# Kernel optimization log

Hardware: AMD Instinct MI355X
Metric: run time of the kernel (lower is better)

Reference implementation:

```python
import jax, jax.numpy as jnp
import numpy as np

EPS = 1e-12
SIMILARITY = 'dot'  # non-tensor forward arg, closed over


def setup_inputs() -> dict:
    key = jax.random.key(0)
    k1, k2, k3, k4 = jax.random.split(key, 4)
    N, M, D = 4096, 8192, 512
    x = jax.random.normal(k1, (N, D), dtype=jnp.float32)
    x_n = jax.random.normal(k2, (M, D), dtype=jnp.float32)
    # Linear(D, 3) params
    W = jax.random.normal(k3, (3, D), dtype=jnp.float32) * (1.0 / np.sqrt(D))
    bias = jax.random.normal(k4, (3,), dtype=jnp.float32) * 0.01
    return {"x": x, "x_n": x_n, "W": W, "bias": bias}


def _sim_matrix(x, x_n, similarity):
    if similarity == 'l2':
        d2 = (jnp.sum(x * x, 1)[:, None] - 2.0 * (x @ x_n.T)
              + jnp.sum(x_n * x_n, 1)[None, :])
        return -jnp.sqrt(jnp.maximum(d2, 0.0))
    elif similarity == 'l1':
        return -jnp.sum(jnp.abs(x[:, None, :] - x_n[None, :, :]), axis=-1)
    elif similarity == 'dot':
        return (x @ x_n.T) / x.shape[1]
    elif similarity == 'cos':
        xn = x / jnp.linalg.norm(x, axis=1, keepdims=True)
        yn = x_n / jnp.linalg.norm(x_n, axis=1, keepdims=True)
        return xn @ yn.T


def reference(x, x_n, W, bias):
    # pointwise params from a Linear(D,3)+Sigmoid head, clamped to (eps, 1-eps)
    p = jnp.clip(jax.nn.sigmoid(x @ W.T + bias), EPS, 1.0 - EPS)  # [N,3]
    a = p[:, 0:1]
    b = p[:, 1:2]
    s = p[:, 2:3]
    b = a + b * (1.0 - a)

    sim = _sim_matrix(x, x_n, SIMILARITY)                # [N,M]
    smin = jnp.min(sim, axis=1, keepdims=True)
    smax = jnp.max(sim, axis=1, keepdims=True)
    sim_norm = (sim - smin) / (smax - smin)

    # x != x_n -> plain row max (torch.equal branch is False)
    top_sims = jnp.max(sim_norm, axis=1, keepdims=True)  # [N,1]
    a = jnp.minimum(a, top_sims) - EPS

    num = jnp.maximum(jnp.abs(sim_norm - a) ** (1.0 / s), EPS)
    denom = num + jnp.maximum(jnp.abs(b - sim_norm) ** (1.0 / s), EPS)
    soft_mask = num / denom

    lo = sim_norm < a
    hi = sim_norm > b
    soft_mask = jnp.where(lo, 0.0, jnp.where(hi, 1.0, soft_mask))
    # safe log: masked-to-0 entries give -inf forward, zero grad (matches torch)
    safe = jnp.where(lo, 1.0, soft_mask)
    log_mask = jnp.where(lo, -jnp.inf, jnp.log(safe))
    return sim + log_mask
```

## Files before the change

### kernel.cpp

```cpp
#include <hip/hip_runtime.h>
#include <hip/hip_fp16.h>
#include <math.h>

#define EPSF 1e-12f
#define NEG_HUGE (-1e30f)

typedef _Float16 half8_t __attribute__((ext_vector_type(8)));
typedef _Float16 half4_t __attribute__((ext_vector_type(4)));
typedef float floatx4 __attribute__((ext_vector_type(4)));

__device__ __forceinline__ float sigmoid_stable(float v) {
    if (v >= 0.0f) {
        return 1.0f / (1.0f + expf(-v));
    } else {
        float e = expf(v);
        return e / (1.0f + e);
    }
}

__global__ __launch_bounds__(64) void row_params_kernel(
    const float* __restrict__ x, const float* __restrict__ W,
    const float* __restrict__ bias,
    float* __restrict__ aeff, float* __restrict__ bnew, float* __restrict__ tinv)
{
    const int r = blockIdx.x;
    const int l = threadIdx.x;
    const float* xr = x + (size_t)r * 512;
    float s0 = 0.0f, s1 = 0.0f, s2 = 0.0f;
#pragma unroll
    for (int i = 0; i < 8; ++i) {
        int e = l * 8 + i;
        float xv = xr[e];
        s0 = fmaf(xv, W[e], s0);
        s1 = fmaf(xv, W[512 + e], s1);
        s2 = fmaf(xv, W[1024 + e], s2);
    }
#pragma unroll
    for (int off = 32; off > 0; off >>= 1) {
        s0 += __shfl_xor(s0, off);
        s1 += __shfl_xor(s1, off);
        s2 += __shfl_xor(s2, off);
    }
    if (l == 0) {
        float p0 = fminf(fmaxf(sigmoid_stable(s0 + bias[0]), EPSF), 1.0f);
        float p1 = fminf(fmaxf(sigmoid_stable(s1 + bias[1]), EPSF), 1.0f);
        float p2 = fminf(fmaxf(sigmoid_stable(s2 + bias[2]), EPSF), 1.0f);
        float b = p0 + p1 * (1.0f - p0);
        float ae = fminf(p0, 1.0f) - EPSF;
        aeff[r] = ae;
        bnew[r] = b;
        tinv[r] = 1.0f / p2;
    }
}

__global__ __launch_bounds__(256) void split_gates_kernel(
    const float* __restrict__ x, const float* __restrict__ xn,
    const float* __restrict__ W, const float* __restrict__ bias,
    _Float16* __restrict__ A2, _Float16* __restrict__ B2,
    float* __restrict__ aeff, float* __restrict__ bnew, float* __restrict__ tinv)
{
    __shared__ float sred[3][4];
    int idx = blockIdx.x * 256 + threadIdx.x;
    int row = idx >> 7;
    int c = (idx & 127) << 2;
    const float* src;
    _Float16* dst;
    bool isB;
    if (row < 4096) {
        src = x + (size_t)row * 512 + c;
        dst = A2 + (size_t)row * 1536 + c;
        isB = false;
    } else {
        int r = row - 4096;
        src = xn + (size_t)r * 512 + c;
        dst = B2 + (size_t)r * 1536 + c;
        isB = true;
    }
    float4 v = *(const float4*)src;
    _Float16 h0 = (_Float16)v.x, h1 = (_Float16)v.y,
             h2 = (_Float16)v.z, h3 = (_Float16)v.w;
    half4_t hv = {h0, h1, h2, h3};
    half4_t lv = {(_Float16)(v.x - (float)h0), (_Float16)(v.y - (float)h1),
                  (_Float16)(v.z - (float)h2), (_Float16)(v.w - (float)h3)};
    *(half4_t*)(dst) = hv;
    *(half4_t*)(dst + 512)  = isB ? lv : hv;
    *(half4_t*)(dst + 1024) = isB ? hv : lv;

    if (!isB) {
        float s0 = v.x * W[c] + v.y * W[c + 1] + v.z * W[c + 2] + v.w * W[c + 3];
        float s1 = v.x * W[512 + c] + v.y * W[513 + c]
                 + v.z * W[514 + c] + v.w * W[515 + c];
        float s2 = v.x * W[1024 + c] + v.y * W[1025 + c]
                 + v.z * W[1026 + c] + v.w * W[1027 + c];
#pragma unroll
        for (int off = 32; off > 0; off >>= 1) {
            s0 += __shfl_xor(s0, off);
            s1 += __shfl_xor(s1, off);
            s2 += __shfl_xor(s2, off);
        }
        const int w = threadIdx.x >> 6;
        if ((threadIdx.x & 63) == 0) {
            sred[0][w] = s0; sred[1][w] = s1; sred[2][w] = s2;
        }
        __syncthreads();
        if ((threadIdx.x & 127) == 0) {
            const int w0 = threadIdx.x >> 6;
            float t0 = sred[0][w0] + sred[0][w0 + 1];
            float t1 = sred[1][w0] + sred[1][w0 + 1];
            float t2 = sred[2][w0] + sred[2][w0 + 1];
            float p0 = fminf(fmaxf(sigmoid_stable(t0 + bias[0]), EPSF), 1.0f);
            float p1 = fminf(fmaxf(sigmoid_stable(t1 + bias[1]), EPSF), 1.0f);
            float p2 = fminf(fmaxf(sigmoid_stable(t2 + bias[2]), EPSF), 1.0f);
            float b = p0 + p1 * (1.0f - p0);
            aeff[row] = fminf(p0, 1.0f) - EPSF;
            bnew[row] = b;
            tinv[row] = 1.0f / p2;
        }
    }
}

#define VMW_(N) asm volatile("s_waitcnt vmcnt(" #N ")" ::: "memory")
#define VMW(N) VMW_(N)
#define BARR() __builtin_amdgcn_s_barrier()

__device__ __forceinline__ void gload16(const _Float16* g, _Float16* l) {
    __builtin_amdgcn_global_load_lds(
        (const __attribute__((address_space(1))) unsigned int*)g,
        (__attribute__((address_space(3))) unsigned int*)l, 16, 0, 0);
}

#define RD_A4(dst, QQ, qd)                                                      \
    dst[0] = *(const half8_t*)(lds + (QQ)*16384 + ArdW + (2*(qd))*1024 + g0);   \
    dst[1] = *(const half8_t*)(lds + (QQ)*16384 + ArdW + (2*(qd))*1024 + g1);   \
    dst[2] = *(const half8_t*)(lds + (QQ)*16384 + ArdW + (2*(qd)+1)*1024 + g0); \
    dst[3] = *(const half8_t*)(lds + (QQ)*16384 + ArdW + (2*(qd)+1)*1024 + g1);

#define RD_B8(dst, QQ)                                                          \
    _Pragma("unroll")                                                           \
    for (int fn = 0; fn < 4; ++fn) {                                            \
        dst[2*fn]   = *(const half8_t*)(lds + (QQ)*16384 + BrdW + fn*1024 + g0);\
        dst[2*fn+1] = *(const half8_t*)(lds + (QQ)*16384 + BrdW + fn*1024 + g1);\
    }

#define MFMA_Q(qd, af, bf)                                                      \
    __builtin_amdgcn_s_setprio(1);                                              \
    _Pragma("unroll")                                                           \
    for (int fn = 0; fn < 4; ++fn) {                                            \
        acc[2*(qd)][fn] = __builtin_amdgcn_mfma_f32_16x16x32_f16(               \
            af[0], bf[2*fn], acc[2*(qd)][fn], 0, 0, 0);                         \
        acc[2*(qd)+1][fn] = __builtin_amdgcn_mfma_f32_16x16x32_f16(             \
            af[2], bf[2*fn], acc[2*(qd)+1][fn], 0, 0, 0);                       \
    }                                                                           \
    _Pragma("unroll")                                                           \
    for (int fn = 0; fn < 4; ++fn) {                                            \
        acc[2*(qd)][fn] = __builtin_amdgcn_mfma_f32_16x16x32_f16(               \
            af[1], bf[2*fn+1], acc[2*(qd)][fn], 0, 0, 0);                       \
        acc[2*(qd)+1][fn] = __builtin_amdgcn_mfma_f32_16x16x32_f16(             \
            af[3], bf[2*fn+1], acc[2*(qd)+1][fn], 0, 0, 0);                     \
    }                                                                           \
    __builtin_amdgcn_s_setprio(0);

__global__ __launch_bounds__(512, 2) void mfma_gemm256_kernel(
    const _Float16* __restrict__ A, const _Float16* __restrict__ B,
    float* __restrict__ C,
    float* __restrict__ pmin, float* __restrict__ pmax)
{
    constexpr int KP = 1536;
    constexpr int NN = 8192;
    __shared__ __align__(16) _Float16 lds[65536];

    const int tid = threadIdx.x;
    const int wave = tid >> 6, lane = tid & 63;
    const int bx = blockIdx.x;
    const int by = blockIdx.y;
    const int wm = (wave >> 2) * 128;
    const int wn = (wave & 3) * 64;

    const int rl = lane & 15, lq = lane >> 4;
    const int rx7 = lane & 7;
    const int lrow = lane >> 3, gph = lane & 7;
    const int glog = gph ^ lrow;

    const _Float16* Bg = B + (size_t)(bx * 256 + wave * 8 + lrow) * KP + glog * 8;
    const _Float16* Ag = A + (size_t)(by * 256 + ((wave & 4) ? 128 : 0)
                                      + (wave & 3) * 8 + lrow) * KP + glog * 8;
    const int BdstW = 32768 + (wave * 8) * 64;
    const int AdstW = (((wave & 4) ? 128 : 0) + (wave & 3) * 8) * 64;
    const int ArdW = (wm + rl) * 64;
    const int BrdW = 32768 + (wn + rl) * 64;
    const int g0 = (lq ^ rx7) * 8;
    const int g1 = ((4 + lq) ^ rx7) * 8;

    floatx4 acc[8][4] = {};
    half8_t a0[4], a1[4], bA[8], bB[8];

    auto stageB = [&](int u, int qn, int kn) {
        gload16(Bg + (size_t)u * (64 * KP) + kn * 64,
                lds + qn * 16384 + BdstW + u * 4096);
    };
    auto stageA = [&](int s, int qn, int kn) {
        gload16(Ag + (size_t)s * (32 * KP) + kn * 64,
                lds + qn * 16384 + AdstW + s * 2048);
    };

#pragma unroll
    for (int u = 0; u < 4; ++u) stageB(u, 0, 0);
#pragma unroll
    for (int s = 0; s < 4; ++s) stageA(s, 0, 0);
    VMW(3);
    BARR();
    RD_B8(bA, 0); RD_A4(a0, 0, 0);
    stageB(0, 1, 1); stageB(1, 1, 1);
    VMW(4);
    BARR();

    for (int kt = 0; kt < 22; kt += 2) {
        const int k1 = kt + 1, k2 = kt + 2, k3 = kt + 3;
        RD_A4(a1, 0, 1); stageB(2, 1, k1); stageB(3, 1, k1);
        MFMA_Q(0, a0, bA); VMW(5); BARR();
        RD_A4(a0, 0, 2); stageA(0, 1, k1); stageA(1, 1, k1);
        MFMA_Q(1, a1, bA); VMW(6); BARR();
        RD_A4(a1, 0, 3); stageA(2, 1, k1); stageA(3, 1, k1);
        MFMA_Q(2, a0, bA); VMW(3); BARR();
        RD_B8(bB, 1); RD_A4(a0, 1, 0); stageB(0, 0, k2); stageB(1, 0, k2);
        MFMA_Q(3, a1, bA); VMW(4); BARR();
        RD_A4(a1, 1, 1); stageB(2, 0, k2); stageB(3, 0, k2);
        MFMA_Q(0, a0, bB); VMW(5); BARR();
        RD_A4(a0, 1, 2); stageA(0, 0, k2); stageA(1, 0, k2);
        MFMA_Q(1, a1, bB); VMW(6); BARR();
        RD_A4(a1, 1, 3); stageA(2, 0, k2); stageA(3, 0, k2);
        MFMA_Q(2, a0, bB); VMW(3); BARR();
        RD_B8(bA, 0); RD_A4(a0, 0, 0); stageB(0, 1, k3); stageB(1, 1, k3);
        MFMA_Q(3, a1, bB); VMW(4); BARR();
    }

    RD_A4(a1, 0, 1); stageB(2, 1, 23); stageB(3, 1, 23);
    MFMA_Q(0, a0, bA); VMW(5); BARR();
    RD_A4(a0, 0, 2); stageA(0, 1, 23); stageA(1, 1, 23);
    MFMA_Q(1, a1, bA); VMW(6); BARR();
    RD_A4(a1, 0, 3); stageA(2, 1, 23); stageA(3, 1, 23);
    MFMA_Q(2, a0, bA); VMW(3); BARR();
    RD_B8(bB, 1); RD_A4(a0, 1, 0);
    MFMA_Q(3, a1, bA); VMW(2); BARR();
    RD_A4(a1, 1, 1); MFMA_Q(0, a0, bB); VMW(1); BARR();
    RD_A4(a0, 1, 2); MFMA_Q(1, a1, bB); VMW(0); BARR();
    RD_A4(a1, 1, 3); MFMA_Q(2, a0, bB);
    MFMA_Q(3, a1, bB);

    const float sc = 1.0f / 512.0f;
    const int row0 = by * 256 + wm + lq * 4;
    const int col0 = bx * 256 + wn + rl;
    const int pslot = bx * 4 + (wave & 3);
#pragma unroll
    for (int fm = 0; fm < 8; ++fm) {
        float mn[4], mx[4];
#pragma unroll
        for (int r = 0; r < 4; ++r) {
            float* cp = C + (size_t)(row0 + fm * 16 + r) * NN + col0;
            float v0 = acc[fm][0][r] * sc, v1 = acc[fm][1][r] * sc;
            float v2 = acc[fm][2][r] * sc, v3 = acc[fm][3][r] * sc;
            cp[0] = v0; cp[16] = v1; cp[32] = v2; cp[48] = v3;
            mn[r] = fminf(fminf(v0, v1), fminf(v2, v3));
            mx[r] = fmaxf(fmaxf(v0, v1), fmaxf(v2, v3));
        }
#pragma unroll
        for (int off = 1; off < 16; off <<= 1)
#pragma unroll
            for (int r = 0; r < 4; ++r) {
                mn[r] = fminf(mn[r], __shfl_xor(mn[r], off));
                mx[r] = fmaxf(mx[r], __shfl_xor(mx[r], off));
            }
        if (rl == 0) {
#pragma unroll
            for (int r = 0; r < 4; ++r) {
                size_t row = (size_t)(row0 + fm * 16 + r);
                pmin[(row << 7) + pslot] = mn[r];
                pmax[(row << 7) + pslot] = mx[r];
            }
        }
    }
}

__device__ __forceinline__ float fast_pow(float x, float t) {
    return __expf(t * __logf(x));
}

__global__ __launch_bounds__(256) void epilogue_row_kernel(
    float* __restrict__ C,
    const float* __restrict__ aeff, const float* __restrict__ bnew,
    const float* __restrict__ tinv,
    const float* __restrict__ pmin, const float* __restrict__ pmax)
{
    const int r = blockIdx.x;
    const int t = threadIdx.x;
    __shared__ float smn[4], smx[4];
    float mn = INFINITY, mx = -INFINITY;
    if (t < 128) {
        mn = pmin[((size_t)r << 7) + t];
        mx = pmax[((size_t)r << 7) + t];
    }
#pragma unroll
    for (int off = 32; off > 0; off >>= 1) {
        mn = fminf(mn, __shfl_xor(mn, off));
        mx = fmaxf(mx, __shfl_xor(mx, off));
    }
    if ((t & 63) == 0) { smn[t >> 6] = mn; smx[t >> 6] = mx; }
    __syncthreads();
    const float rmn = fminf(smn[0], smn[1]);
    const float rmx = fmaxf(smx[0], smx[1]);

    const float a = aeff[r];
    const float b = bnew[r];
    const float tv = tinv[r];
    const float range = rmx - rmn;
    const float inv_range = (range > 0.0f) ? (1.0f / range) : 0.0f;

    floatx4* prow = (floatx4*)(C + (size_t)r * 8192);
#pragma unroll
    for (int i = 0; i < 8; ++i) {
        floatx4* p = prow + t + i * 256;
        floatx4 v = __builtin_nontemporal_load(p);
        floatx4 out;
#pragma unroll
        for (int j = 0; j < 4; ++j) {
            float sim = v[j];
            float sn = (sim - rmn) * inv_range;
            float lm;
            if (sn < a) {
                lm = NEG_HUGE;
            } else if (sn > b) {
                lm = 0.0f;
            } else {
                float num = fmaxf(fast_pow(fabsf(sn - a), tv), EPSF);
                float den = num + fmaxf(fast_pow(fabsf(b - sn), tv), EPSF);
                lm = __logf(num / den);
            }
            out[j] = sim + lm;
        }
        __builtin_nontemporal_store(out, p);
    }
}

#define BM 128
#define BN 128
#define BK 16
__global__ __launch_bounds__(256) void sgemm_nt_kernel(
    const float* __restrict__ A, const float* __restrict__ B,
    float* __restrict__ C)
{
    const int K = 512;
    const int N = 8192;
    __shared__ float As[BK][BM];
    __shared__ float Bs[BK][BN];
    const int t = threadIdx.x;
    const int bx = blockIdx.x, by = blockIdx.y;
    const int m0 = t >> 2;
    const int kq = (t & 3) << 2;
    const float* Ap = A + ((size_t)(by * BM + m0) * K + kq);
    const float* Bp = B + ((size_t)(bx * BN + m0) * K + kq);
    const int tx = t & 15, ty = t >> 4;
    float acc[8][8] = {};
    float4 a0 = *(const float4*)(Ap), a1 = *(const float4*)(Ap + (size_t)64 * K);
    float4 b0 = *(const float4*)(Bp), b1 = *(const float4*)(Bp + (size_t)64 * K);
    for (int kt = 0; kt < K / BK; ++kt) {
        As[kq + 0][m0] = a0.x; As[kq + 1][m0] = a0.y; As[kq + 2][m0] = a0.z; As[kq + 3][m0] = a0.w;
        As[kq + 0][m0 + 64] = a1.x; As[kq + 1][m0 + 64] = a1.y; As[kq + 2][m0 + 64] = a1.z; As[kq + 3][m0 + 64] = a1.w;
        Bs[kq + 0][m0] = b0.x; Bs[kq + 1][m0] = b0.y; Bs[kq + 2][m0] = b0.z; Bs[kq + 3][m0] = b0.w;
        Bs[kq + 0][m0 + 64] = b1.x; Bs[kq + 1][m0 + 64] = b1.y; Bs[kq + 2][m0 + 64] = b1.z; Bs[kq + 3][m0 + 64] = b1.w;
        __syncthreads();
        if (kt + 1 < K / BK) {
            const float* Ap2 = Ap + (size_t)(kt + 1) * BK;
            const float* Bp2 = Bp + (size_t)(kt + 1) * BK;
            a0 = *(const float4*)(Ap2); a1 = *(const float4*)(Ap2 + (size_t)64 * K);
            b0 = *(const float4*)(Bp2); b1 = *(const float4*)(Bp2 + (size_t)64 * K);
        }
#pragma unroll
        for (int k = 0; k < BK; ++k) {
            float4 xa0 = *(const float4*)(&As[k][ty * 8]);
            float4 xa1 = *(const float4*)(&As[k][ty * 8 + 4]);
            float4 yb0 = *(const float4*)(&Bs[k][tx * 8]);
            float4 yb1 = *(const float4*)(&Bs[k][tx * 8 + 4]);
            float av[8] = {xa0.x, xa0.y, xa0.z, xa0.w, xa1.x, xa1.y, xa1.z, xa1.w};
            float bv[8] = {yb0.x, yb0.y, yb0.z, yb0.w, yb1.x, yb1.y, yb1.z, yb1.w};
#pragma unroll
            for (int i = 0; i < 8; ++i)
#pragma unroll
                for (int j = 0; j < 8; ++j)
                    acc[i][j] = fmaf(av[i], bv[j], acc[i][j]);
        }
        __syncthreads();
    }
    const float sc = 1.0f / 512.0f;
    const int gm = by * BM + ty * 8, gn = bx * BN + tx * 8;
#pragma unroll
    for (int i = 0; i < 8; ++i) {
        float4 o0 = make_float4(acc[i][0] * sc, acc[i][1] * sc, acc[i][2] * sc, acc[i][3] * sc);
        float4 o1 = make_float4(acc[i][4] * sc, acc[i][5] * sc, acc[i][6] * sc, acc[i][7] * sc);
        float* cp = C + (size_t)(gm + i) * N + gn;
        *(float4*)(cp) = o0;
        *(float4*)(cp + 4) = o1;
    }
}

__global__ __launch_bounds__(256) void row_minmax_kernel(
    const float* __restrict__ C, float* __restrict__ smin, float* __restrict__ smax)
{
    const int r = blockIdx.x;
    const float4* row = (const float4*)(C + (size_t)r * 8192);
    float mn = INFINITY, mx = -INFINITY;
#pragma unroll
    for (int i = 0; i < 8; ++i) {
        float4 v = row[threadIdx.x + i * 256];
        mn = fminf(mn, fminf(fminf(v.x, v.y), fminf(v.z, v.w)));
        mx = fmaxf(mx, fmaxf(fmaxf(v.x, v.y), fmaxf(v.z, v.w)));
    }
#pragma unroll
    for (int off = 32; off > 0; off >>= 1) {
        mn = fminf(mn, __shfl_xor(mn, off));
        mx = fmaxf(mx, __shfl_xor(mx, off));
    }
    __shared__ float smn[4], smx[4];
    if ((threadIdx.x & 63) == 0) {
        smn[threadIdx.x >> 6] = mn;
        smx[threadIdx.x >> 6] = mx;
    }
    __syncthreads();
    if (threadIdx.x == 0) {
        mn = fminf(fminf(smn[0], smn[1]), fminf(smn[2], smn[3]));
        mx = fmaxf(fmaxf(smx[0], smx[1]), fmaxf(smx[2], smx[3]));
        smin[r] = mn;
        smax[r] = mx;
    }
}

__global__ __launch_bounds__(256) void epilogue_kernel(
    float* __restrict__ C,
    const float* __restrict__ aeff, const float* __restrict__ bnew,
    const float* __restrict__ tinv,
    const float* __restrict__ smin, const float* __restrict__ smax)
{
    const int r = blockIdx.y;
    const int c4 = blockIdx.x * 256 + threadIdx.x;
    const float a = aeff[r];
    const float b = bnew[r];
    const float t = tinv[r];
    const float mn = smin[r];
    const float range = smax[r] - mn;
    const float inv_range = (range > 0.0f) ? (1.0f / range) : 0.0f;

    floatx4* p = (floatx4*)(C + (size_t)r * 8192) + c4;
    floatx4 v = __builtin_nontemporal_load(p);
    floatx4 out;
#pragma unroll
    for (int i = 0; i < 4; ++i) {
        float sim = v[i];
        float sn = (sim - mn) * inv_range;
        float lm;
        if (sn < a) {
            lm = NEG_HUGE;
        } else if (sn > b) {
            lm = 0.0f;
        } else {
            float num = fmaxf(fast_pow(fabsf(sn - a), t), EPSF);
            float den = num + fmaxf(fast_pow(fabsf(b - sn), t), EPSF);
            lm = __logf(num / den);
        }
        out[i] = sim + lm;
    }
    __builtin_nontemporal_store(out, p);
}

extern "C" void kernel_launch(void* const* d_in, const int* in_sizes, int n_in,
                              void* d_out, int out_size, void* d_ws, size_t ws_size,
                              hipStream_t stream)
{
    const float* x    = (const float*)d_in[0];
    const float* x_n  = (const float*)d_in[1];
    const float* W    = (const float*)d_in[2];
    const float* bias = (const float*)d_in[3];
    float* C = (float*)d_out;
    float* ws = (float*)d_ws;

    float* aeff = ws;
    float* bnew = ws + 4096;
    float* tinv = ws + 8192;
    float* smin = ws + 12288;
    float* smax = ws + 16384;

    const size_t pmin_off = 128 * 1024;
    const size_t pbytes = (size_t)4096 * 128 * 4;
    const size_t a2_off = pmin_off + 2 * pbytes;
    const size_t a2_bytes = (size_t)4096 * 1536 * 2;
    const size_t b2_off = a2_off + a2_bytes;
    const size_t need = b2_off + (size_t)8192 * 1536 * 2;

    if (ws_size >= need) {
        float* pmin = (float*)((char*)d_ws + pmin_off);
        float* pmax = (float*)((char*)d_ws + pmin_off + pbytes);
        _Float16* A2 = (_Float16*)((char*)d_ws + a2_off);
        _Float16* B2 = (_Float16*)((char*)d_ws + b2_off);
        split_gates_kernel<<<6144, 256, 0, stream>>>(x, x_n, W, bias, A2, B2,
                                                     aeff, bnew, tinv);
        mfma_gemm256_kernel<<<dim3(32, 16), 512, 0, stream>>>(A2, B2, C, pmin, pmax);
        epilogue_row_kernel<<<4096, 256, 0, stream>>>(C, aeff, bnew, tinv,
                                                      pmin, pmax);
    } else {
        row_params_kernel<<<4096, 64, 0, stream>>>(x, W, bias, aeff, bnew, tinv);
        sgemm_nt_kernel<<<dim3(8192 / BN, 4096 / BM), 256, 0, stream>>>(x, x_n, C);
        row_minmax_kernel<<<4096, 256, 0, stream>>>(C, smin, smax);
        epilogue_kernel<<<dim3(8, 4096), 256, 0, stream>>>(C, aeff, bnew, tinv,
                                                           smin, smax);
    }
}
```

Before: 293.9 us.

## Restructure GEMM main loop with single fragment buffers and explicit LDS waits

Result: no change. 296.0 us (+0.7%).

```diff
diff --git a/kernel.cpp b/kernel.cpp
--- a/kernel.cpp
+++ b/kernel.cpp
@@ -122,6 +122,8 @@
 #define VMW_(N) asm volatile("s_waitcnt vmcnt(" #N ")" ::: "memory")
 #define VMW(N) VMW_(N)
 #define BARR() __builtin_amdgcn_s_barrier()
+#define LGKM0() asm volatile("s_waitcnt lgkmcnt(0)" ::: "memory")
+#define LGKM8() asm volatile("s_waitcnt lgkmcnt(8)" ::: "memory")
 
 __device__ __forceinline__ void gload16(const _Float16* g, _Float16* l) {
     __builtin_amdgcn_global_load_lds(
@@ -192,7 +194,7 @@
     const int g1 = ((4 + lq) ^ rx7) * 8;
 
     floatx4 acc[8][4] = {};
-    half8_t a0[4], a1[4], bA[8], bB[8];
+    half8_t af[4], bfr[8];
 
     auto stageB = [&](int u, int qn, int kn) {
         gload16(Bg + (size_t)u * (64 * KP) + kn * 64,
@@ -207,45 +209,56 @@
     for (int u = 0; u < 4; ++u) stageB(u, 0, 0);
 #pragma unroll
     for (int s = 0; s < 4; ++s) stageA(s, 0, 0);
-    VMW(3);
-    BARR();
-    RD_B8(bA, 0); RD_A4(a0, 0, 0);
-    stageB(0, 1, 1); stageB(1, 1, 1);
-    VMW(4);
+#pragma unroll
+    for (int u = 0; u < 4; ++u) stageB(u, 1, 1);
+    stageA(0, 1, 1); stageA(1, 1, 1);
+    VMW(6);
     BARR();
 
     for (int kt = 0; kt < 22; kt += 2) {
         const int k1 = kt + 1, k2 = kt + 2, k3 = kt + 3;
-        RD_A4(a1, 0, 1); stageB(2, 1, k1); stageB(3, 1, k1);
-        MFMA_Q(0, a0, bA); VMW(5); BARR();
-        RD_A4(a0, 0, 2); stageA(0, 1, k1); stageA(1, 1, k1);
-        MFMA_Q(1, a1, bA); VMW(6); BARR();
-        RD_A4(a1, 0, 3); stageA(2, 1, k1); stageA(3, 1, k1);
-        MFMA_Q(2, a0, bA); VMW(3); BARR();
-        RD_B8(bB, 1); RD_A4(a0, 1, 0); stageB(0, 0, k2); stageB(1, 0, k2);
-        MFMA_Q(3, a1, bA); VMW(4); BARR();
-        RD_A4(a1, 1, 1); stageB(2, 0, k2); stageB(3, 0, k2);
-        MFMA_Q(0, a0, bB); VMW(5); BARR();
-        RD_A4(a0, 1, 2); stageA(0, 0, k2); stageA(1, 0, k2);
-        MFMA_Q(1, a1, bB); VMW(6); BARR();
-        RD_A4(a1, 1, 3); stageA(2, 0, k2); stageA(3, 0, k2);
-        MFMA_Q(2, a0, bB); VMW(3); BARR();
-        RD_B8(bA, 0); RD_A4(a0, 0, 0); stageB(0, 1, k3); stageB(1, 1, k3);
-        MFMA_Q(3, a1, bB); VMW(4); BARR();
-    }
-
-    RD_A4(a1, 0, 1); stageB(2, 1, 23); stageB(3, 1, 23);
-    MFMA_Q(0, a0, bA); VMW(5); BARR();
-    RD_A4(a0, 0, 2); stageA(0, 1, 23); stageA(1, 1, 23);
-    MFMA_Q(1, a1, bA); VMW(6); BARR();
-    RD_A4(a1, 0, 3); stageA(2, 1, 23); stageA(3, 1, 23);
-    MFMA_Q(2, a0, bA); VMW(3); BARR();
-    RD_B8(bB, 1); RD_A4(a0, 1, 0);
-    MFMA_Q(3, a1, bA); VMW(2); BARR();
-    RD_A4(a1, 1, 1); MFMA_Q(0, a0, bB); VMW(1); BARR();
-    RD_A4(a0, 1, 2); MFMA_Q(1, a1, bB); VMW(0); BARR();
-    RD_A4(a1, 1, 3); MFMA_Q(2, a0, bB);
-    MFMA_Q(3, a1, bB);
+        RD_B8(bfr, 0); RD_A4(af, 0, 0); stageA(2, 1, k1); stageA(3, 1, k1);
+        LGKM8(); BARR(); LGKM0();
+        MFMA_Q(0, af, bfr); BARR();
+        RD_A4(af, 0, 1); stageB(0, 0, k2); stageB(1, 0, k2);
+        BARR(); LGKM0();
+        MFMA_Q(1, af, bfr); BARR();
+        RD_A4(af, 0, 2); stageB(2, 0, k2); stageB(3, 0, k2);
+        BARR(); LGKM0();
+        MFMA_Q(2, af, bfr); BARR();
+        RD_A4(af, 0, 3); stageA(0, 0, k2); stageA(1, 0, k2);
+        BARR(); LGKM0();
+        MFMA_Q(3, af, bfr); VMW(6); BARR();
+        RD_B8(bfr, 1); RD_A4(af, 1, 0); stageA(2, 0, k2); stageA(3, 0, k2);
+        LGKM8(); BARR(); LGKM0();
+        MFMA_Q(0, af, bfr); BARR();
+        RD_A4(af, 1, 1); stageB(0, 1, k3); stageB(1, 1, k3);
+        BARR(); LGKM0();
+        MFMA_Q(1, af, bfr); BARR();
+        RD_A4(af, 1, 2); stageB(2, 1, k3); stageB(3, 1, k3);
+        BARR(); LGKM0();
+        MFMA_Q(2, af, bfr); BARR();
+        RD_A4(af, 1, 3); stageA(0, 1, k3); stageA(1, 1, k3);
+        BARR(); LGKM0();
+        MFMA_Q(3, af, bfr); VMW(6); BARR();
+    }
+
+    RD_B8(bfr, 0); RD_A4(af, 0, 0); stageA(2, 1, 23); stageA(3, 1, 23);
+    LGKM8(); BARR(); LGKM0(); MFMA_Q(0, af, bfr); BARR();
+    RD_A4(af, 0, 1);
+    BARR(); LGKM0(); MFMA_Q(1, af, bfr); BARR();
+    RD_A4(af, 0, 2);
+    BARR(); LGKM0(); MFMA_Q(2, af, bfr); BARR();
+    RD_A4(af, 0, 3);
+    BARR(); LGKM0(); MFMA_Q(3, af, bfr); VMW(0); BARR();
+    RD_B8(bfr, 1); RD_A4(af, 1, 0);
+    LGKM8(); BARR(); LGKM0(); MFMA_Q(0, af, bfr); BARR();
+    RD_A4(af, 1, 1);
+    BARR(); LGKM0(); MFMA_Q(1, af, bfr); BARR();
+    RD_A4(af, 1, 2);
+    BARR(); LGKM0(); MFMA_Q(2, af, bfr); BARR();
+    RD_A4(af, 1, 3);
+    LGKM0(); MFMA_Q(3, af, bfr);
 
     const float sc = 1.0f / 512.0f;
     const int row0 = by * 256 + wm + lq * 4;
```
